# Optimization experiments

Hardware: AMD Instinct MI355X
Metric: run time of the kernel (lower is better)

## Reference

```python
import jax, jax.numpy as jnp
import numpy as np

DIM = 2048
N_HEADS = 16
N_KV_HEADS = 8
HEAD_DIM = DIM // N_HEADS  # 128
N_REP = N_HEADS // N_KV_HEADS  # 2
B, L = 2, 2048
ROPE_THETA = 10000.0


def make_freqs_cis(L, head_dim, theta):
    inv = 1.0 / (theta ** (np.arange(0, head_dim, 2, dtype=np.float32) / head_dim))
    t = np.arange(L, dtype=np.float32)
    ang = np.outer(t, inv)  # [L, head_dim//2]
    return jnp.asarray(np.stack([np.cos(ang), np.sin(ang)], axis=-1))  # [L, hd//2, 2]


def setup_inputs() -> dict:
    key = jax.random.key(0)
    ks = jax.random.split(key, 5)
    s = 1.0 / np.sqrt(DIM)
    return {
        "x": jax.random.normal(ks[0], (B, L, DIM), dtype=jnp.float32),
        "freqs_cis": make_freqs_cis(L, HEAD_DIM, ROPE_THETA),
        "wq": jax.random.normal(ks[1], (DIM, N_HEADS * HEAD_DIM), dtype=jnp.float32) * s,
        "wk": jax.random.normal(ks[2], (DIM, N_KV_HEADS * HEAD_DIM), dtype=jnp.float32) * s,
        "wv": jax.random.normal(ks[3], (DIM, N_KV_HEADS * HEAD_DIM), dtype=jnp.float32) * s,
        "wo": jax.random.normal(ks[4], (N_HEADS * HEAD_DIM, DIM), dtype=jnp.float32) * s,
    }


def apply_rotary(x, freqs_cis):
    # x: [B, L, H, D]; freqs_cis: [L, D//2, 2] (cos, sin)
    xr = x.reshape(*x.shape[:-1], -1, 2)  # [B,L,H,D//2,2]
    cos = freqs_cis[None, :, None, :, 0]
    sin = freqs_cis[None, :, None, :, 1]
    out_r = xr[..., 0] * cos - xr[..., 1] * sin
    out_i = xr[..., 0] * sin + xr[..., 1] * cos
    return jnp.stack([out_r, out_i], axis=-1).reshape(x.shape).astype(x.dtype)


def reference(x, freqs_cis, wq, wk, wv, wo):
    Bx, Lx, _ = x.shape
    xq = (x @ wq).reshape(Bx, Lx, N_HEADS, HEAD_DIM)
    xk = (x @ wk).reshape(Bx, Lx, N_KV_HEADS, HEAD_DIM)
    xv = (x @ wv).reshape(Bx, Lx, N_KV_HEADS, HEAD_DIM)
    xq = apply_rotary(xq, freqs_cis)
    xk = apply_rotary(xk, freqs_cis)
    # repeat kv heads (GQA) then put heads first: [B, H, L, D]
    keys = jnp.repeat(xk, N_REP, axis=2).transpose(0, 2, 1, 3)
    values = jnp.repeat(xv, N_REP, axis=2).transpose(0, 2, 1, 3)
    xq = xq.transpose(0, 2, 1, 3)
    scores = jnp.einsum("bhqd,bhkd->bhqk", xq, keys) / jnp.sqrt(
        jnp.asarray(HEAD_DIM, dtype=xq.dtype))
    causal = jnp.tril(jnp.ones((Lx, Lx), dtype=bool))
    scores = jnp.where(causal[None, None], scores, -jnp.inf)
    probs = jax.nn.softmax(scores.astype(jnp.float32), axis=-1).astype(xq.dtype)
    out = jnp.einsum("bhqk,bhkd->bhqd", probs, values)
    out = out.transpose(0, 2, 1, 3).reshape(Bx, Lx, -1)
    return out @ wo
```

## Files before the change

### kernel.cpp

```cpp
#include <hip/hip_runtime.h>
#include <math.h>

typedef unsigned short u16;
typedef unsigned int   u32;
typedef u16   u16x8 __attribute__((ext_vector_type(8)));
typedef u16   u16x4 __attribute__((ext_vector_type(4)));
typedef u16   u16x2 __attribute__((ext_vector_type(2)));
typedef __bf16 bf16x8 __attribute__((ext_vector_type(8)));
typedef float  f32x4 __attribute__((ext_vector_type(4)));

__device__ __forceinline__ u16 f2b(float f) {
    union { float f; u32 u; } v; v.f = f;
    u32 u = v.u;
    return (u16)((u + 0x7FFFu + ((u >> 16) & 1u)) >> 16);
}

__device__ __forceinline__ void glds16(const void* g, void* l) {
    __builtin_amdgcn_global_load_lds(
        (__attribute__((address_space(1))) void*)(void*)g,
        (__attribute__((address_space(3))) void*)l, 16, 0, 0);
}

__global__ __launch_bounds__(256) void convert_f32_bf16(
    const float* __restrict__ src, u16* __restrict__ dst)
{
    const size_t i = ((size_t)blockIdx.x * 256 + threadIdx.x) * 8;
    f32x4 a = *(const f32x4*)&src[i];
    f32x4 b = *(const f32x4*)&src[i + 4];
    u16x8 o;
    #pragma unroll
    for (int j = 0; j < 4; ++j) { o[j] = f2b(a[j]); o[4 + j] = f2b(b[j]); }
    *(u16x8*)&dst[i] = o;
}

__global__ __launch_bounds__(256) void transpose_f32_bf16(
    const float* __restrict__ src, u16* __restrict__ dst, int R, int C)
{
    __shared__ u16 tile[64 * 72];
    const int t = threadIdx.x;
    const int r0 = blockIdx.y * 64, c0 = blockIdx.x * 64;
    #pragma unroll
    for (int i = 0; i < 2; ++i) {
        int idx = i * 256 + t;
        int r = idx >> 3, c8 = (idx & 7) * 8;
        const float* sp = &src[(size_t)(r0 + r) * C + c0 + c8];
        f32x4 a = *(const f32x4*)sp;
        f32x4 b = *(const f32x4*)(sp + 4);
        u16x8 v;
        #pragma unroll
        for (int j = 0; j < 4; ++j) { v[j] = f2b(a[j]); v[4 + j] = f2b(b[j]); }
        *(u16x8*)&tile[r * 72 + c8] = v;
    }
    __syncthreads();
    #pragma unroll
    for (int i = 0; i < 2; ++i) {
        int idx = i * 256 + t;
        int orow = idx >> 3, oc8 = (idx & 7) * 8;
        u16x8 w;
        #pragma unroll
        for (int j = 0; j < 8; ++j) w[j] = tile[(oc8 + j) * 72 + orow];
        *(u16x8*)&dst[(size_t)(c0 + orow) * R + r0 + oc8] = w;
    }
}

template <int MODE>
__global__ __launch_bounds__(512, 2) void gemm_bt(
    const u16* __restrict__ A, const u16* __restrict__ Bt,
    u16* __restrict__ D0, u16* __restrict__ D1, u16* __restrict__ D2,
    float* __restrict__ Fout, const float* __restrict__ fc)
{
    __shared__ u16 SA[2][16384];
    __shared__ u16 SB[2][16384];
    const int t = threadIdx.x;
    const int w = t >> 6, lane = t & 63;
    const int l15 = lane & 15, qd = lane >> 4;

    const int nwg = gridDim.x * gridDim.y;
    const int lin = blockIdx.y * gridDim.x + blockIdx.x;
    const int swz = (lin & 7) * (nwg >> 3) + (lin >> 3);
    const int bx = swz % gridDim.x, by = swz / gridDim.x;
    const int row0 = by * 256, col0 = bx * 256;

    const int wmf = (w >> 2) * 8;
    const int wnf = (w & 3) * 4;

#define STAGE_A(dst, k0, sel) do {                                            \
    { const int mf = ((w >> 2) * 8) + (sel) * 4 + (w & 3);                    \
      glds16(A + (size_t)(row0 + mf * 16 + l15) * 2048 + (k0) + qd * 8,       \
             (dst) + (mf * 2 + 0) * 512); }                                   \
    { const int mf = ((w >> 2) * 8) + (sel) * 4 + (w & 3);                    \
      glds16(A + (size_t)(row0 + mf * 16 + l15) * 2048 + (k0) + 32 + qd * 8,  \
             (dst) + (mf * 2 + 1) * 512); }                                   \
} while (0)
#define STAGE_B(dst, k0, sel) do {                                            \
    { const int nf = ((w >> 1) * 4) + (sel) * 2 + (w & 1);                    \
      glds16(Bt + (size_t)(col0 + nf * 16 + l15) * 2048 + (k0) + qd * 8,      \
             (dst) + (nf * 2 + 0) * 512); }                                   \
    { const int nf = ((w >> 1) * 4) + (sel) * 2 + (w & 1);                    \
      glds16(Bt + (size_t)(col0 + nf * 16 + l15) * 2048 + (k0) + 32 + qd * 8, \
             (dst) + (nf * 2 + 1) * 512); }                                   \
} while (0)
#define FENCE asm volatile("" ::: "memory")
#define VMW(n) asm volatile("s_waitcnt vmcnt(" #n ")" ::: "memory")

    f32x4 acc[8][4] = {};
    bf16x8 af[4][2], bfr[4][2];

    STAGE_A(&SA[0][0], 0, 0);
    STAGE_B(&SB[0][0], 0, 0);
    STAGE_B(&SB[0][0], 0, 1);
    STAGE_A(&SA[0][0], 0, 1);
    VMW(4);
    FENCE; __builtin_amdgcn_s_barrier();

    for (int kt = 0; kt < 32; ++kt) {
        const int par = kt & 1;
        const u16* Ac = &SA[par][0];
        const u16* Bc = &SB[par][0];
        u16* An = &SA[par ^ 1][0];
        u16* Bn = &SB[par ^ 1][0];
        const int nk0 = (kt + 1) * 64;
        const bool st = (kt < 31);

        #pragma unroll
        for (int mf = 0; mf < 4; ++mf)
            #pragma unroll
            for (int ks = 0; ks < 2; ++ks)
                af[mf][ks] = *(const bf16x8*)&Ac[((wmf + mf) * 2 + ks) * 512 + lane * 8];
        #pragma unroll
        for (int nf = 0; nf < 2; ++nf)
            #pragma unroll
            for (int ks = 0; ks < 2; ++ks)
                bfr[nf][ks] = *(const bf16x8*)&Bc[((wnf + nf) * 2 + ks) * 512 + lane * 8];
        if (st) STAGE_A(An, nk0, 0);
        __builtin_amdgcn_s_setprio(1);
        #pragma unroll
        for (int mf = 0; mf < 4; ++mf)
            #pragma unroll
            for (int nf = 0; nf < 2; ++nf)
                #pragma unroll
                for (int ks = 0; ks < 2; ++ks)
                    acc[mf][nf] = __builtin_amdgcn_mfma_f32_16x16x32_bf16(
                        af[mf][ks], bfr[nf][ks], acc[mf][nf], 0, 0, 0);
        __builtin_amdgcn_s_setprio(0);
        if (st) { VMW(4); } else { VMW(2); }
        FENCE; __builtin_amdgcn_s_barrier();

        #pragma unroll
        for (int nf = 0; nf < 2; ++nf)
            #pragma unroll
            for (int ks = 0; ks < 2; ++ks)
                bfr[2 + nf][ks] = *(const bf16x8*)&Bc[((wnf + 2 + nf) * 2 + ks) * 512 + lane * 8];
        if (st) STAGE_B(Bn, nk0, 0);
        __builtin_amdgcn_s_setprio(1);
        #pragma unroll
        for (int mf = 0; mf < 4; ++mf)
            #pragma unroll
            for (int nf = 0; nf < 2; ++nf)
                #pragma unroll
                for (int ks = 0; ks < 2; ++ks)
                    acc[mf][2 + nf] = __builtin_amdgcn_mfma_f32_16x16x32_bf16(
                        af[mf][ks], bfr[2 + nf][ks], acc[mf][2 + nf], 0, 0, 0);
        __builtin_amdgcn_s_setprio(0);
        if (st) { VMW(4); } else { VMW(0); }
        FENCE; __builtin_amdgcn_s_barrier();

        #pragma unroll
        for (int mf = 0; mf < 4; ++mf)
            #pragma unroll
            for (int ks = 0; ks < 2; ++ks)
                af[mf][ks] = *(const bf16x8*)&Ac[((wmf + 4 + mf) * 2 + ks) * 512 + lane * 8];
        if (st) STAGE_B(Bn, nk0, 1);
        __builtin_amdgcn_s_setprio(1);
        #pragma unroll
        for (int mf = 0; mf < 4; ++mf)
            #pragma unroll
            for (int nf = 0; nf < 2; ++nf)
                #pragma unroll
                for (int ks = 0; ks < 2; ++ks)
                    acc[4 + mf][2 + nf] = __builtin_amdgcn_mfma_f32_16x16x32_bf16(
                        af[mf][ks], bfr[2 + nf][ks], acc[4 + mf][2 + nf], 0, 0, 0);
        __builtin_amdgcn_s_setprio(0);
        FENCE; __builtin_amdgcn_s_barrier();

        if (st) STAGE_A(An, nk0, 1);
        __builtin_amdgcn_s_setprio(1);
        #pragma unroll
        for (int mf = 0; mf < 4; ++mf)
            #pragma unroll
            for (int nf = 0; nf < 2; ++nf)
                #pragma unroll
                for (int ks = 0; ks < 2; ++ks)
                    acc[4 + mf][nf] = __builtin_amdgcn_mfma_f32_16x16x32_bf16(
                        af[mf][ks], bfr[nf][ks], acc[4 + mf][nf], 0, 0, 0);
        __builtin_amdgcn_s_setprio(0);
        if (st) { VMW(4); }
        FENCE; __builtin_amdgcn_s_barrier();
    }
#undef STAGE_A
#undef STAGE_B
#undef FENCE
#undef VMW

    #pragma unroll
    for (int mt = 0; mt < 8; ++mt)
        #pragma unroll
        for (int nt = 0; nt < 4; ++nt) {
            const int gcol = col0 + (w & 3) * 64 + nt * 16 + l15;
            const int grow0 = row0 + (w >> 2) * 128 + mt * 16 + qd * 4;
            if (MODE == 1) {
                #pragma unroll
                for (int r = 0; r < 4; ++r)
                    Fout[(size_t)(grow0 + r) * 2048 + gcol] = acc[mt][nt][r];
            } else if (gcol >= 3072) {
                const int vcol = gcol - 3072;
                const int vrow = vcol + (grow0 >> 11) * 1024;
                u16x4 v;
                #pragma unroll
                for (int r = 0; r < 4; ++r) v[r] = f2b(acc[mt][nt][r]);
                *(u16x4*)&D2[(size_t)vrow * 2048 + (grow0 & 2047)] = v;
            } else {
                const int p2 = gcol & 126;
                #pragma unroll
                for (int r = 0; r < 4; ++r) {
                    const int l = (grow0 + r) & 2047;
                    const float c = fc[l * 128 + p2];
                    const float s = fc[l * 128 + p2 + 1];
                    const float own = acc[mt][nt][r];
                    const float oth = __shfl_xor(own, 1);
                    const float rot = (l15 & 1) ? (oth * s + own * c)
                                                : (own * c - oth * s);
                    const u16 v = f2b(rot);
                    if (gcol < 2048)
                        D0[(size_t)(grow0 + r) * 2048 + gcol] = v;
                    else
                        D1[(size_t)(grow0 + r) * 1024 + (gcol - 2048)] = v;
                }
            }
        }
}

__global__ __launch_bounds__(256, 2) void attn_kernel(
    const u16* __restrict__ Q, const u16* __restrict__ K,
    const u16* __restrict__ Vt, u16* __restrict__ AO)
{
    __shared__ u16 SM[32768];
    const int t = threadIdx.x;
    const int w = t >> 6, lane = t & 63;
    const int l15 = lane & 15, qd = lane >> 4;
    const int b = blockIdx.x >> 3, kvh = blockIdx.x & 7;
    const int y = (int)blockIdx.y;
    const int qt = (y < 16) ? (31 - y) : (y - 16);
    const int h = kvh * 2 + (w >> 1);
    const float SCL = 0.08838834764831845f * 1.4426950408889634f;

    u16* K0 = SM;
    u16* K1 = SM + 8192;
    u16* VB = SM + 16384;
    u16* PW = SM + 24576 + w * 2048;

    bf16x8 qf[2][4];
    #pragma unroll
    for (int mt = 0; mt < 2; ++mt) {
        const size_t grow = (size_t)b * 2048 + qt * 64 + (w & 1) * 32 + mt * 16 + l15;
        const u16* qp = Q + grow * 2048 + h * 128 + qd * 8;
        #pragma unroll
        for (int ks = 0; ks < 4; ++ks)
            qf[mt][ks] = *(const bf16x8*)(qp + ks * 32);
    }
    f32x4 Oa[2][8] = {};
    f32x4 Ls[2] = {};
    bf16x8 onesv;
    #pragma unroll
    for (int j = 0; j < 8; ++j) onesv[j] = (__bf16)1.0f;

    const u16* Kbase = K  + (size_t)b * 2048 * 1024 + kvh * 128;
    const u16* Vbase = Vt + (size_t)(b * 8 + kvh) * 128 * 2048;

    #pragma unroll
    for (int j = 0; j < 4; ++j) {
        const int f = w * 4 + j;
        glds16(Kbase + (size_t)((f >> 2) * 16 + l15) * 1024 + ((f & 3) * 4 + qd) * 8,
               K0 + f * 512);
    }
    __syncthreads();

    for (int kt = 0; kt <= qt; ++kt) {
        u16* Kc = (kt & 1) ? K1 : K0;
        u16* Kn = (kt & 1) ? K0 : K1;
        if (kt < qt) {
            #pragma unroll
            for (int j = 0; j < 4; ++j) {
                const int f = w * 4 + j;
                glds16(Kbase + (size_t)((kt + 1) * 64 + (f >> 2) * 16 + l15) * 1024
                             + ((f & 3) * 4 + qd) * 8,
                       Kn + f * 512);
            }
        }
        #pragma unroll
        for (int j = 0; j < 4; ++j) {
            const int f = w * 4 + j;
            glds16(Vbase + (size_t)((f >> 1) * 16 + l15) * 2048 + kt * 64
                         + ((f & 1) * 4 + qd) * 8,
                   VB + f * 512);
        }

        f32x4 S[2][4] = {};
        #pragma unroll
        for (int ks = 0; ks < 4; ++ks) {
            bf16x8 bk[4];
            #pragma unroll
            for (int nt = 0; nt < 4; ++nt)
                bk[nt] = *(const bf16x8*)&Kc[(nt * 4 + ks) * 512 + lane * 8];
            __builtin_amdgcn_s_setprio(1);
            #pragma unroll
            for (int mt = 0; mt < 2; ++mt)
                #pragma unroll
                for (int nt = 0; nt < 4; ++nt)
                    S[mt][nt] = __builtin_amdgcn_mfma_f32_16x16x32_bf16(
                        qf[mt][ks], bk[nt], S[mt][nt], 0, 0, 0);
            __builtin_amdgcn_s_setprio(0);
        }
        if (kt == qt) {
            #pragma unroll
            for (int mt = 0; mt < 2; ++mt)
                #pragma unroll
                for (int r = 0; r < 4; ++r) {
                    const int qg = (w & 1) * 32 + mt * 16 + qd * 4 + r;
                    #pragma unroll
                    for (int nt = 0; nt < 4; ++nt)
                        if (nt * 16 + l15 > qg) S[mt][nt][r] = -__builtin_inff();
                }
        }
        #pragma unroll
        for (int mt = 0; mt < 2; ++mt)
            #pragma unroll
            for (int nt = 0; nt < 4; ++nt)
                #pragma unroll
                for (int r = 0; r < 4; ++r) {
                    const float p = exp2f(S[mt][nt][r] * SCL - 12.0f);
                    PW[(mt * 2 + (nt >> 1)) * 512 + ((nt * 2 + (l15 >> 3)) & 3) * 128
                       + (qd * 4 + r) * 8 + (l15 & 7)] = f2b(p);
                }

        __syncthreads();

        #pragma unroll
        for (int ks = 0; ks < 2; ++ks) {
            bf16x8 pa[2], vb[8];
            #pragma unroll
            for (int mt = 0; mt < 2; ++mt)
                pa[mt] = *(const bf16x8*)&PW[(mt * 2 + ks) * 512 + lane * 8];
            #pragma unroll
            for (int nt = 0; nt < 8; ++nt)
                vb[nt] = *(const bf16x8*)&VB[(nt * 2 + ks) * 512 + lane * 8];
            __builtin_amdgcn_s_setprio(1);
            #pragma unroll
            for (int mt = 0; mt < 2; ++mt) {
                Ls[mt] = __builtin_amdgcn_mfma_f32_16x16x32_bf16(
                    pa[mt], onesv, Ls[mt], 0, 0, 0);
                #pragma unroll
                for (int nt = 0; nt < 8; ++nt)
                    Oa[mt][nt] = __builtin_amdgcn_mfma_f32_16x16x32_bf16(
                        pa[mt], vb[nt], Oa[mt][nt], 0, 0, 0);
            }
            __builtin_amdgcn_s_setprio(0);
        }
        __syncthreads();
    }

    u16* OL = SM;
    #pragma unroll
    for (int mt = 0; mt < 2; ++mt)
        #pragma unroll
        for (int r = 0; r < 4; ++r) {
            const float inv = 1.f / Ls[mt][r];
            const int qr = (w & 1) * 32 + mt * 16 + qd * 4 + r;
            #pragma unroll
            for (int nt = 0; nt < 8; ++nt)
                OL[qr * 256 + (w >> 1) * 128 + nt * 16 + l15] = f2b(Oa[mt][nt][r] * inv);
        }
    __syncthreads();
    #pragma unroll
    for (int i = 0; i < 8; ++i) {
        const int c = i * 256 + t;
        const int row = c >> 5, ch = c & 31;
        u16x8 v = *(const u16x8*)&OL[row * 256 + ch * 8];
        *(u16x8*)&AO[((size_t)b * 2048 + qt * 64 + row) * 2048 + kvh * 256 + ch * 8] = v;
    }
}

extern "C" void kernel_launch(void* const* d_in, const int* in_sizes, int n_in,
                              void* d_out, int out_size, void* d_ws, size_t ws_size,
                              hipStream_t stream)
{
    (void)in_sizes; (void)n_in; (void)out_size; (void)ws_size;
    const float* x  = (const float*)d_in[0];
    const float* fc = (const float*)d_in[1];
    const float* wq = (const float*)d_in[2];
    const float* wk = (const float*)d_in[3];
    const float* wv = (const float*)d_in[4];
    const float* wo = (const float*)d_in[5];
    float* out = (float*)d_out;
    char* ws = (char*)d_ws;

    u16* Qb  = (u16*)(ws);
    u16* Kb  = (u16*)(ws + 16777216);
    u16* Vt  = (u16*)(ws + 25165824);
    u16* Xb  = (u16*)(ws + 33554432);
    u16* AO  = (u16*)(ws + 33554432);
    u16* WT  = (u16*)(ws + 50331648);
    u16* WOT = (u16*)(ws + 67108864);

    convert_f32_bf16<<<4096, 256, 0, stream>>>(x, Xb);
    transpose_f32_bf16<<<dim3(32, 32), 256, 0, stream>>>(wq, WT, 2048, 2048);
    transpose_f32_bf16<<<dim3(16, 32), 256, 0, stream>>>(wk, WT + 2048 * 2048, 2048, 1024);
    transpose_f32_bf16<<<dim3(16, 32), 256, 0, stream>>>(wv, WT + 3072 * 2048, 2048, 1024);
    transpose_f32_bf16<<<dim3(32, 32), 256, 0, stream>>>(wo, WOT, 2048, 2048);

    gemm_bt<0><<<dim3(16, 16), 512, 0, stream>>>(Xb, WT, Qb, Kb, Vt, nullptr, fc);

    attn_kernel<<<dim3(16, 32), 256, 0, stream>>>(Qb, Kb, Vt, AO);

    gemm_bt<1><<<dim3(8, 16), 512, 0, stream>>>(AO, WOT, nullptr, nullptr, nullptr, out, nullptr);
}
```

Before: 284.4 us.

## Deepen GEMM global-to-LDS prefetch to two K-tiles ahead

```diff
diff --git a/kernel.cpp b/kernel.cpp
--- a/kernel.cpp
+++ b/kernel.cpp
@@ -84,55 +84,46 @@
     const int wmf = (w >> 2) * 8;
     const int wnf = (w & 3) * 4;
 
-#define STAGE_A(dst, k0, sel) do {                                            \
-    { const int mf = ((w >> 2) * 8) + (sel) * 4 + (w & 3);                    \
-      glds16(A + (size_t)(row0 + mf * 16 + l15) * 2048 + (k0) + qd * 8,       \
-             (dst) + (mf * 2 + 0) * 512); }                                   \
-    { const int mf = ((w >> 2) * 8) + (sel) * 4 + (w & 3);                    \
-      glds16(A + (size_t)(row0 + mf * 16 + l15) * 2048 + (k0) + 32 + qd * 8,  \
-             (dst) + (mf * 2 + 1) * 512); }                                   \
+#define STAGE_A_HALF(par, h, kt) do {                                         \
+    const int f_ = (h) * 8 + w;                                               \
+    const u16* g_ = A + (size_t)(row0 + f_ * 16 + l15) * 2048                 \
+                      + (kt) * 64 + qd * 8;                                   \
+    glds16(g_,      &SA[par][(f_ * 2 + 0) * 512]);                            \
+    glds16(g_ + 32, &SA[par][(f_ * 2 + 1) * 512]);                            \
 } while (0)
-#define STAGE_B(dst, k0, sel) do {                                            \
-    { const int nf = ((w >> 1) * 4) + (sel) * 2 + (w & 1);                    \
-      glds16(Bt + (size_t)(col0 + nf * 16 + l15) * 2048 + (k0) + qd * 8,      \
-             (dst) + (nf * 2 + 0) * 512); }                                   \
-    { const int nf = ((w >> 1) * 4) + (sel) * 2 + (w & 1);                    \
-      glds16(Bt + (size_t)(col0 + nf * 16 + l15) * 2048 + (k0) + 32 + qd * 8, \
-             (dst) + (nf * 2 + 1) * 512); }                                   \
+#define STAGE_B_HALF(par, h, kt) do {                                         \
+    const int f_ = (h) * 8 + w;                                               \
+    const u16* g_ = Bt + (size_t)(col0 + f_ * 16 + l15) * 2048                \
+                       + (kt) * 64 + qd * 8;                                  \
+    glds16(g_,      &SB[par][(f_ * 2 + 0) * 512]);                            \
+    glds16(g_ + 32, &SB[par][(f_ * 2 + 1) * 512]);                            \
 } while (0)
 #define FENCE asm volatile("" ::: "memory")
-#define VMW(n) asm volatile("s_waitcnt vmcnt(" #n ")" ::: "memory")
 
     f32x4 acc[8][4] = {};
     bf16x8 af[4][2], bfr[4][2];
 
-    STAGE_A(&SA[0][0], 0, 0);
-    STAGE_B(&SB[0][0], 0, 0);
-    STAGE_B(&SB[0][0], 0, 1);
-    STAGE_A(&SA[0][0], 0, 1);
-    VMW(4);
+    STAGE_A_HALF(0, 0, 0); STAGE_B_HALF(0, 0, 0);
+    STAGE_A_HALF(0, 1, 0); STAGE_B_HALF(0, 1, 0);
+    STAGE_A_HALF(1, 0, 1); STAGE_B_HALF(1, 0, 1);
+    STAGE_A_HALF(1, 1, 1);
+    asm volatile("s_waitcnt vmcnt(6)" ::: "memory");
     FENCE; __builtin_amdgcn_s_barrier();
 
     for (int kt = 0; kt < 32; ++kt) {
-        const int par = kt & 1;
-        const u16* Ac = &SA[par][0];
-        const u16* Bc = &SB[par][0];
-        u16* An = &SA[par ^ 1][0];
-        u16* Bn = &SB[par ^ 1][0];
-        const int nk0 = (kt + 1) * 64;
-        const bool st = (kt < 31);
+        const int par = kt & 1, nx = par ^ 1;
 
         #pragma unroll
         for (int mf = 0; mf < 4; ++mf)
             #pragma unroll
             for (int ks = 0; ks < 2; ++ks)
-                af[mf][ks] = *(const bf16x8*)&Ac[((wmf + mf) * 2 + ks) * 512 + lane * 8];
+                af[mf][ks] = *(const bf16x8*)&SA[par][((wmf + mf) * 2 + ks) * 512 + lane * 8];
         #pragma unroll
         for (int nf = 0; nf < 2; ++nf)
             #pragma unroll
             for (int ks = 0; ks < 2; ++ks)
-                bfr[nf][ks] = *(const bf16x8*)&Bc[((wnf + nf) * 2 + ks) * 512 + lane * 8];
-        if (st) STAGE_A(An, nk0, 0);
+                bfr[nf][ks] = *(const bf16x8*)&SB[par][((wnf + nf) * 2 + ks) * 512 + lane * 8];
+        if (kt < 31) STAGE_B_HALF(nx, 1, kt + 1);
         __builtin_amdgcn_s_setprio(1);
         #pragma unroll
         for (int mf = 0; mf < 4; ++mf)
@@ -143,15 +134,13 @@
                     acc[mf][nf] = __builtin_amdgcn_mfma_f32_16x16x32_bf16(
                         af[mf][ks], bfr[nf][ks], acc[mf][nf], 0, 0, 0);
         __builtin_amdgcn_s_setprio(0);
-        if (st) { VMW(4); } else { VMW(2); }
         FENCE; __builtin_amdgcn_s_barrier();
 
         #pragma unroll
         for (int nf = 0; nf < 2; ++nf)
             #pragma unroll
             for (int ks = 0; ks < 2; ++ks)
-                bfr[2 + nf][ks] = *(const bf16x8*)&Bc[((wnf + 2 + nf) * 2 + ks) * 512 + lane * 8];
-        if (st) STAGE_B(Bn, nk0, 0);
+                bfr[2 + nf][ks] = *(const bf16x8*)&SB[par][((wnf + 2 + nf) * 2 + ks) * 512 + lane * 8];
         __builtin_amdgcn_s_setprio(1);
         #pragma unroll
         for (int mf = 0; mf < 4; ++mf)
@@ -162,15 +151,13 @@
                     acc[mf][2 + nf] = __builtin_amdgcn_mfma_f32_16x16x32_bf16(
                         af[mf][ks], bfr[2 + nf][ks], acc[mf][2 + nf], 0, 0, 0);
         __builtin_amdgcn_s_setprio(0);
-        if (st) { VMW(4); } else { VMW(0); }
         FENCE; __builtin_amdgcn_s_barrier();
 
         #pragma unroll
         for (int mf = 0; mf < 4; ++mf)
             #pragma unroll
             for (int ks = 0; ks < 2; ++ks)
-                af[mf][ks] = *(const bf16x8*)&Ac[((wmf + 4 + mf) * 2 + ks) * 512 + lane * 8];
-        if (st) STAGE_B(Bn, nk0, 1);
+                af[mf][ks] = *(const bf16x8*)&SA[par][((wmf + 4 + mf) * 2 + ks) * 512 + lane * 8];
         __builtin_amdgcn_s_setprio(1);
         #pragma unroll
         for (int mf = 0; mf < 4; ++mf)
@@ -183,7 +170,11 @@
         __builtin_amdgcn_s_setprio(0);
         FENCE; __builtin_amdgcn_s_barrier();
 
-        if (st) STAGE_A(An, nk0, 1);
+        if (kt < 30) {
+            STAGE_A_HALF(par, 0, kt + 2);
+            STAGE_B_HALF(par, 0, kt + 2);
+            STAGE_A_HALF(par, 1, kt + 2);
+        }
         __builtin_amdgcn_s_setprio(1);
         #pragma unroll
         for (int mf = 0; mf < 4; ++mf)
@@ -194,13 +185,13 @@
                     acc[4 + mf][nf] = __builtin_amdgcn_mfma_f32_16x16x32_bf16(
                         af[mf][ks], bfr[nf][ks], acc[4 + mf][nf], 0, 0, 0);
         __builtin_amdgcn_s_setprio(0);
-        if (st) { VMW(4); }
+        if (kt < 30) asm volatile("s_waitcnt vmcnt(6)" ::: "memory");
+        else         asm volatile("s_waitcnt vmcnt(0)" ::: "memory");
         FENCE; __builtin_amdgcn_s_barrier();
     }
-#undef STAGE_A
-#undef STAGE_B
+#undef STAGE_A_HALF
+#undef STAGE_B_HALF
 #undef FENCE
-#undef VMW
 
     #pragma unroll
     for (int mt = 0; mt < 8; ++mt)
```

After: 295.6 us. +3.9%, slower.
